# Optimization experiments

Measured on AMD Instinct MI355X. Metric: run time of the kernel, lower is better.

The kernel has to match this reference:

```python
import jax, jax.numpy as jnp
import numpy as np

E = 23   # unique_experts_num
K = 3    # act_experts_num
D = 1024 # in_features
H = 768  # hidden_features (0.75 * dim, per MOEBlock mlp_ratio)


def setup_inputs() -> dict:
    key = jax.random.key(0)
    ks = jax.random.split(key, 12)
    s_in = 1.0 / np.sqrt(D)
    s_hid = 1.0 / np.sqrt(H)
    x = jax.random.normal(ks[0], (4, 1024, D), dtype=jnp.float32)
    gate_W = jax.random.normal(ks[1], (D, E), dtype=jnp.float32) * s_in
    gate_b = jnp.zeros((E,), jnp.float32)
    bias = jnp.zeros((E,), jnp.float32)  # registered buffer, init to zeros
    W1 = jax.random.normal(ks[2], (E, D, H), dtype=jnp.float32) * s_in
    b1 = jnp.zeros((E, H), jnp.float32)
    W2 = jax.random.normal(ks[3], (E, H, D), dtype=jnp.float32) * s_hid
    b2 = jnp.zeros((E, D), jnp.float32)
    sW1 = jax.random.normal(ks[4], (D, H), dtype=jnp.float32) * s_in
    sb1 = jnp.zeros((H,), jnp.float32)
    sW2 = jax.random.normal(ks[5], (H, D), dtype=jnp.float32) * s_hid
    sb2 = jnp.zeros((D,), jnp.float32)
    return {"x": x, "gate_W": gate_W, "gate_b": gate_b, "bias": bias,
            "W1": W1, "b1": b1, "W2": W2, "b2": b2,
            "sW1": sW1, "sb1": sb1, "sW2": sW2, "sb2": sb2}


def reference(x, gate_W, gate_b, bias, W1, b1, W2, b2, sW1, sb1, sW2, sb2):
    o_shape = x.shape
    xt = x.reshape(-1, o_shape[-1])          # [T, D]
    T = xt.shape[0]

    # gating: sigmoid gate, top-k indices chosen on (gate + bias), weights gathered from gate
    gate = jax.nn.sigmoid(xt @ gate_W + gate_b)            # [T, E]
    _, top_idx = jax.lax.top_k(gate + bias, K)             # [T, K]
    top_w = jnp.take_along_axis(gate, top_idx, axis=-1)    # [T, K]
    top_w = top_w / jnp.sum(top_w, axis=-1, keepdims=True)

    # combine matrix: C[t, e] = normalized gate weight if e in top-k of token t else 0
    C = jnp.zeros((T, E), xt.dtype).at[jnp.arange(T)[:, None], top_idx].set(top_w)

    # all-expert dense compute (math-equivalent to dispatch/compute/combine)
    h = jax.nn.gelu(jnp.einsum('td,edh->eth', xt, W1) + b1[:, None, :], approximate=False)
    y = jnp.einsum('eth,ehd->etd', h, W2) + b2[:, None, :]  # [E, T, D]
    moe_out = jnp.einsum('etd,te->td', y, C)                # weighted combine

    # shared expert applied to every token
    shared = jax.nn.gelu(xt @ sW1 + sb1, approximate=False) @ sW2 + sb2
    out = shared + moe_out

    # aux load-balance loss
    gate_norm = gate / jnp.sum(gate, axis=-1, keepdims=True)
    P = jnp.mean(gate_norm, axis=0)                          # [E]
    counts = jnp.sum(jax.nn.one_hot(top_idx, E, dtype=jnp.float32), axis=(0, 1))  # [E]
    F = E * counts / (K * T)
    aux_loss = jnp.sum(P * F)

    return out.reshape(o_shape), aux_loss, counts.astype(jnp.int32)
```

## Files before the change

### kernel.cpp

```cpp
#include <hip/hip_runtime.h>
#include <math.h>

#define TT 4096
#define DD 1024
#define HH 768
#define NE 23
#define NG 24
#define BM 128
#define BN 128
#define BK 64
#define MAXT 160
#define KB1 16
#define KB2 12
#define NY1 6
#define NY2 8
#define NWG1 (MAXT*NY1)
#define NWG2 (MAXT*NY2)

#define WS_CURS   0
#define WS_COUNTS 512
#define WS_PSUM   544
#define WS_OFFS   576
#define WS_TOFFS  608
#define WS_TOTAL  640
#define WS_T2E    672
#define WS_T2A    832
#define WS_TOKE   1024
#define WS_TOKW   13312
#define WS_LTOK   25600
#define WS_LW     41984
#define WS_PPART  58368
#define WS_CPART  81920
#define WS_SIDX   106496
#define XB_OFF  ((size_t)524288)
#define H_OFF   ((size_t)8912896)
#define W1B_OFF ((size_t)34078720)
#define W2B_OFF ((size_t)71827456)

typedef short bf16x8 __attribute__((ext_vector_type(8)));
typedef float f32x4 __attribute__((ext_vector_type(4)));
typedef unsigned short u16x8 __attribute__((ext_vector_type(8)));

#define S_BARRIER() asm volatile("s_barrier" ::: "memory")
#define WAIT_VM8()  asm volatile("s_waitcnt vmcnt(8)" ::: "memory")
#define WAIT_VM0()  asm volatile("s_waitcnt vmcnt(0)" ::: "memory")

__device__ inline unsigned short bfr(float f) {
    unsigned u = __float_as_uint(f);
    u += 0x7fffu + ((u >> 16) & 1u);
    return (unsigned short)(u >> 16);
}
__device__ inline float b2f(unsigned short u) {
    return __uint_as_float((unsigned)u << 16);
}

__device__ __forceinline__ void gl_lds16(const void* g, void* l) {
    __builtin_amdgcn_global_load_lds(
        (const __attribute__((address_space(1))) unsigned int*)g,
        (__attribute__((address_space(3))) unsigned int*)l, 16, 0, 0);
}

__global__ __launch_bounds__(256) void k_gate(
    const float* __restrict__ x, const float* __restrict__ gW,
    const float* __restrict__ gb, const float* __restrict__ bias,
    int* __restrict__ tokE, float* __restrict__ tokW,
    float* __restrict__ Ppart, int* __restrict__ Cpart)
{
    __shared__ float xs[4][DD];
    __shared__ float gv[4][NE];
    __shared__ float ginvs[4];
    __shared__ int sel[4][3];
    const int tid = threadIdx.x;
    const int t0 = blockIdx.x * 4;
    {
        const float4* src = (const float4*)(x + (size_t)t0 * DD);
        float4* dst = (float4*)&xs[0][0];
        #pragma unroll
        for (int i = 0; i < 4; i++) dst[tid + 256 * i] = src[tid + 256 * i];
    }
    __syncthreads();
    const int w = tid >> 6, l = tid & 63;
    const int t = t0 + w;
    if (l < NE) {
        float s0 = 0.f, s1 = 0.f, s2 = 0.f, s3 = 0.f;
        const float* xw = xs[w];
        for (int d = 0; d < DD; d += 4) {
            s0 = fmaf(xw[d + 0], gW[(d + 0) * NE + l], s0);
            s1 = fmaf(xw[d + 1], gW[(d + 1) * NE + l], s1);
            s2 = fmaf(xw[d + 2], gW[(d + 2) * NE + l], s2);
            s3 = fmaf(xw[d + 3], gW[(d + 3) * NE + l], s3);
        }
        float s = (s0 + s1) + (s2 + s3) + gb[l];
        gv[w][l] = 1.f / (1.f + expf(-s));
    }
    __syncthreads();
    if (l == 0) {
        unsigned chosen = 0;
        int be[3]; float bw[3];
        float gsum = 0.f;
        for (int e = 0; e < NE; e++) gsum += gv[w][e];
        #pragma unroll
        for (int k = 0; k < 3; k++) {
            float m = -1e30f; int mi = 0;
            for (int e = 0; e < NE; e++) {
                float kv = gv[w][e] + bias[e];
                if (!((chosen >> e) & 1u) && kv > m) { m = kv; mi = e; }
            }
            chosen |= 1u << mi;
            be[k] = mi; bw[k] = gv[w][mi];
        }
        float inv = 1.f / (bw[0] + bw[1] + bw[2]);
        #pragma unroll
        for (int k = 0; k < 3; k++) {
            tokE[t * 3 + k] = be[k];
            tokW[t * 3 + k] = bw[k] * inv;
            sel[w][k] = be[k];
        }
        ginvs[w] = 1.f / gsum;
    }
    __syncthreads();
    if (tid < NE) {
        float p = gv[0][tid] * ginvs[0] + gv[1][tid] * ginvs[1]
                + gv[2][tid] * ginvs[2] + gv[3][tid] * ginvs[3];
        Ppart[tid * 1024 + blockIdx.x] = p;
        int c = 0;
        #pragma unroll
        for (int w2 = 0; w2 < 4; w2++)
            #pragma unroll
            for (int k = 0; k < 3; k++) c += (sel[w2][k] == tid);
        Cpart[tid * 1024 + blockIdx.x] = c;
    }
}

__global__ __launch_bounds__(256) void k_reduce(
    const float* __restrict__ Ppart, const int* __restrict__ Cpart,
    int* __restrict__ counts, float* __restrict__ Psum)
{
    const int e = blockIdx.x;
    const int tid = threadIdx.x;
    float s = 0.f; int c = 0;
    for (int i = tid; i < 1024; i += 256) {
        s += Ppart[e * 1024 + i];
        c += Cpart[e * 1024 + i];
    }
    #pragma unroll
    for (int off = 32; off >= 1; off >>= 1) {
        s += __shfl_down(s, off, 64);
        c += __shfl_down(c, off, 64);
    }
    __shared__ float ss[4]; __shared__ int sc[4];
    if ((tid & 63) == 0) { ss[tid >> 6] = s; sc[tid >> 6] = c; }
    __syncthreads();
    if (tid == 0) {
        Psum[e] = ss[0] + ss[1] + ss[2] + ss[3];
        counts[e] = sc[0] + sc[1] + sc[2] + sc[3];
    }
}

__global__ void k_scan(const int* __restrict__ counts, const float* __restrict__ Psum,
                       int* __restrict__ offs, int* __restrict__ toffs,
                       int* __restrict__ total, int* __restrict__ t2e,
                       int* __restrict__ t2a, float* __restrict__ outAux)
{
    if (threadIdx.x != 0 || blockIdx.x != 0) return;
    int off = 0, toff = 0;
    for (int e = 0; e < NG; e++) {
        int c = (e < NE) ? counts[e] : TT;
        offs[e] = off; toffs[e] = toff;
        int nt = (c + BM - 1) / BM;
        for (int t = 0; t < nt; t++) {
            t2e[toff + t] = e;
            t2a[toff + t] = off + t * BM;
        }
        off += c; toff += nt;
    }
    offs[NG] = off; toffs[NG] = toff;
    *total = toff;
    float aux = 0.f;
    for (int e = 0; e < NE; e++) {
        float P = Psum[e] / (float)TT;
        float F = (float)NE * (float)counts[e] / (float)(3 * TT);
        aux += P * F;
    }
    outAux[0] = aux;
    for (int e = 0; e < NE; e++) outAux[1 + e] = (float)counts[e];
}

__global__ void k_scatter(const int* __restrict__ tokE, const float* __restrict__ tokW,
                          const int* __restrict__ offs, int* __restrict__ curs,
                          int* __restrict__ ltok, float* __restrict__ lw,
                          int* __restrict__ sidx)
{
    int t = blockIdx.x * 256 + threadIdx.x;
    if (t >= TT) return;
    #pragma unroll
    for (int k = 0; k < 3; k++) {
        int e = tokE[t * 3 + k];
        int pos = atomicAdd(&curs[e * 16], 1);
        int idx = offs[e] + pos;
        ltok[idx] = t; lw[idx] = tokW[t * 3 + k];
        sidx[t * 3 + k] = idx;
    }
    ltok[3 * TT + t] = t;
    lw[3 * TT + t] = 1.f;
}

__global__ __launch_bounds__(256) void k_cvt_x(const float* __restrict__ x,
                                               unsigned short* __restrict__ xb)
{
    const int tid = threadIdx.x;
    #pragma unroll
    for (int it = 0; it < 4; it++) {
        int idx = blockIdx.x * 1024 + it * 256 + tid;
        float4 v = ((const float4*)x)[idx];
        ((ushort4*)xb)[idx] = make_ushort4(bfr(v.x), bfr(v.y), bfr(v.z), bfr(v.w));
    }
}

__global__ __launch_bounds__(256) void k_cvt_w(
    const float* __restrict__ W, const float* __restrict__ Ws,
    int K, int N, unsigned short* __restrict__ dst)
{
    const int e = blockIdx.z, kb = blockIdx.y;
    const int KBt = gridDim.y;
    const int n0 = blockIdx.x * 64;
    const float* src = (e < NE) ? (W + (size_t)e * K * N) : Ws;
    __shared__ unsigned short Ls[64][66];
    const int tid = threadIdx.x;
    const int c = (tid & 15) * 4, r0 = tid >> 4;
    #pragma unroll
    for (int pass = 0; pass < 4; pass++) {
        int row = pass * 16 + r0;
        float4 v = *(const float4*)(src + (size_t)(kb * 64 + row) * N + n0 + c);
        ushort4 u = make_ushort4(bfr(v.x), bfr(v.y), bfr(v.z), bfr(v.w));
        *(ushort4*)&Ls[row][c] = u;
    }
    __syncthreads();
    unsigned short* dbase = dst + ((size_t)(e * KBt + kb) * N + n0) * 64;
    #pragma unroll
    for (int half = 0; half < 2; half++) {
        int g = half * 256 + tid;
        int n = g >> 3, p = g & 7;
        int j = p ^ (n & 7);
        u16x8 u;
        #pragma unroll
        for (int i = 0; i < 8; i++) u[i] = Ls[j * 8 + i][n];
        *(u16x8*)(dbase + n * 64 + p * 8) = u;
    }
}

__global__ __launch_bounds__(256) void k_mm1(
    const unsigned short* __restrict__ xb, const unsigned short* __restrict__ W1b,
    const float* __restrict__ b1, const float* __restrict__ sb1,
    const int* __restrict__ t2e, const int* __restrict__ t2a,
    const int* __restrict__ offs, const int* __restrict__ total,
    const int* __restrict__ ltok, unsigned short* __restrict__ H)
{
    const int id = blockIdx.x;
    const int wg = (id & 7) * (NWG1 / 8) + (id >> 3);
    const int ns = wg / MAXT;
    const int tb = wg % MAXT;
    if (tb >= *total) return;
    const int e = t2e[tb];
    const int a0 = t2a[tb];
    const int acount = min(offs[e + 1] - a0, BM);
    const float* bb = (e < NE) ? (b1 + e * HH) : sb1;
    const int nb = ns * BN;

    __shared__ unsigned short As[2][BM * BK];
    __shared__ unsigned short Bs[2][BN * BK];
    __shared__ int rows[BM];
    const int tid = threadIdx.x;
    if (tid < BM) rows[tid] = ltok[a0 + min(tid, acount - 1)];
    __syncthreads();

    const int wid = tid >> 6, lane = tid & 63;
    const int wr = wid >> 1, wc = wid & 1;
    const int l15 = lane & 15, l4 = lane >> 4;

    float bv[4];
    #pragma unroll
    for (int n = 0; n < 4; n++) bv[n] = bb[nb + wc * 64 + n * 16 + l15];

    f32x4 acc[4][4];
    #pragma unroll
    for (int m = 0; m < 4; m++)
        #pragma unroll
        for (int n = 0; n < 4; n++) acc[m][n] = (f32x4){0.f, 0.f, 0.f, 0.f};

    const unsigned short* aSrc[4];
    int Goff[4];
    #pragma unroll
    for (int c = 0; c < 4; c++) {
        int G = (wid * 4 + c) * 64 + lane;
        int row = G >> 3, j = G & 7;
        aSrc[c] = xb + (size_t)rows[row] * DD + ((j ^ (row & 7)) << 3);
        Goff[c] = G * 8;
    }
    const unsigned short* wbase = W1b + ((size_t)e * KB1 * HH + nb) * 64;

    auto stage = [&](int buf, int kb) {
        #pragma unroll
        for (int c = 0; c < 4; c++)
            gl_lds16(aSrc[c] + kb * 64, &As[buf][Goff[c]]);
        const unsigned short* wb = wbase + (size_t)kb * (HH * 64);
        #pragma unroll
        for (int c = 0; c < 4; c++)
            gl_lds16(wb + Goff[c], &Bs[buf][Goff[c]]);
    };
    auto compute = [&](int buf) {
        #pragma unroll
        for (int kh = 0; kh < 2; kh++) {
            bf16x8 af[4], bf[4];
            #pragma unroll
            for (int f = 0; f < 4; f++) {
                int ar = wr * 64 + f * 16 + l15;
                int br = wc * 64 + f * 16 + l15;
                int pg = (kh << 2) + l4;
                af[f] = *(const bf16x8*)&As[buf][ar * 64 + ((pg ^ (ar & 7)) << 3)];
                bf[f] = *(const bf16x8*)&Bs[buf][br * 64 + ((pg ^ (br & 7)) << 3)];
            }
            #pragma unroll
            for (int m = 0; m < 4; m++)
                #pragma unroll
                for (int n = 0; n < 4; n++)
                    acc[m][n] = __builtin_amdgcn_mfma_f32_16x16x32_bf16(af[m], bf[n], acc[m][n], 0, 0, 0);
        }
    };

    stage(0, 0);
    stage(1, 1);
    WAIT_VM8();
    S_BARRIER();
    #pragma unroll 1
    for (int kb = 0; kb < KB1; kb++) {
        const int cur = kb & 1;
        compute(cur);
        S_BARRIER();
        if (kb + 2 < KB1) {
            stage(cur, kb + 2);
            WAIT_VM8();
            S_BARRIER();
        } else if (kb + 1 < KB1) {
            WAIT_VM0();
            S_BARRIER();
        }
    }

    #pragma unroll
    for (int m = 0; m < 4; m++) {
        int rbase = wr * 64 + m * 16 + l4 * 4;
        #pragma unroll
        for (int n = 0; n < 4; n++) {
            int col = nb + wc * 64 + n * 16 + l15;
            #pragma unroll
            for (int i = 0; i < 4; i++) {
                int r = rbase + i;
                if (r < acount) {
                    float v = acc[m][n][i] + bv[n];
                    float g = 0.5f * v * (1.f + erff(v * 0.70710678118f));
                    H[(size_t)(a0 + r) * HH + col] = bfr(g);
                }
            }
        }
    }
}

__global__ __launch_bounds__(256) void k_mm2(
    const unsigned short* __restrict__ H, const unsigned short* __restrict__ W2b,
    const float* __restrict__ b2, const float* __restrict__ sb2,
    const int* __restrict__ t2e, const int* __restrict__ t2a,
    const int* __restrict__ offs, const int* __restrict__ total,
    const int* __restrict__ ltok, const float* __restrict__ lw,
    unsigned short* __restrict__ yslot, float* __restrict__ out)
{
    const int id = blockIdx.x;
    const int wg = (id & 7) * (NWG2 / 8) + (id >> 3);
    const int ns = wg / MAXT;
    const int tb = wg % MAXT;
    if (tb >= *total) return;
    const int e = t2e[tb];
    const int a0 = t2a[tb];
    const int acount = min(offs[e + 1] - a0, BM);
    const float* bb = (e < NE) ? (b2 + e * DD) : sb2;
    const int nb = ns * BN;

    __shared__ unsigned short As[2][BM * BK];
    __shared__ unsigned short Bs[2][BN * BK];
    __shared__ int rows[BM];
    __shared__ float wts[BM];
    const int tid = threadIdx.x;
    if (tid < BM) {
        rows[tid] = (tid < acount) ? ltok[a0 + tid] : -1;
        wts[tid]  = (tid < acount) ? lw[a0 + tid] : 0.f;
    }
    __syncthreads();

    const int wid = tid >> 6, lane = tid & 63;
    const int wr = wid >> 1, wc = wid & 1;
    const int l15 = lane & 15, l4 = lane >> 4;

    float bv[4];
    #pragma unroll
    for (int n = 0; n < 4; n++) bv[n] = bb[nb + wc * 64 + n * 16 + l15];

    f32x4 acc[4][4];
    #pragma unroll
    for (int m = 0; m < 4; m++)
        #pragma unroll
        for (int n = 0; n < 4; n++) acc[m][n] = (f32x4){0.f, 0.f, 0.f, 0.f};

    const unsigned short* aSrc[4];
    int Goff[4];
    #pragma unroll
    for (int c = 0; c < 4; c++) {
        int G = (wid * 4 + c) * 64 + lane;
        int row = G >> 3, j = G & 7;
        aSrc[c] = H + (size_t)(a0 + row) * HH + ((j ^ (row & 7)) << 3);
        Goff[c] = G * 8;
    }
    const unsigned short* wbase = W2b + ((size_t)e * KB2 * DD + nb) * 64;

    auto stage = [&](int buf, int kb) {
        #pragma unroll
        for (int c = 0; c < 4; c++)
            gl_lds16(aSrc[c] + kb * 64, &As[buf][Goff[c]]);
        const unsigned short* wb = wbase + (size_t)kb * (DD * 64);
        #pragma unroll
        for (int c = 0; c < 4; c++)
            gl_lds16(wb + Goff[c], &Bs[buf][Goff[c]]);
    };
    auto compute = [&](int buf) {
        #pragma unroll
        for (int kh = 0; kh < 2; kh++) {
            bf16x8 af[4], bf[4];
            #pragma unroll
            for (int f = 0; f < 4; f++) {
                int ar = wr * 64 + f * 16 + l15;
                int br = wc * 64 + f * 16 + l15;
                int pg = (kh << 2) + l4;
                af[f] = *(const bf16x8*)&As[buf][ar * 64 + ((pg ^ (ar & 7)) << 3)];
                bf[f] = *(const bf16x8*)&Bs[buf][br * 64 + ((pg ^ (br & 7)) << 3)];
            }
            #pragma unroll
            for (int m = 0; m < 4; m++)
                #pragma unroll
                for (int n = 0; n < 4; n++)
                    acc[m][n] = __builtin_amdgcn_mfma_f32_16x16x32_bf16(af[m], bf[n], acc[m][n], 0, 0, 0);
        }
    };

    stage(0, 0);
    stage(1, 1);
    WAIT_VM8();
    S_BARRIER();
    #pragma unroll 1
    for (int kb = 0; kb < KB2; kb++) {
        const int cur = kb & 1;
        compute(cur);
        S_BARRIER();
        if (kb + 2 < KB2) {
            stage(cur, kb + 2);
            WAIT_VM8();
            S_BARRIER();
        } else if (kb + 1 < KB2) {
            WAIT_VM0();
            S_BARRIER();
        }
    }

    if (e == NE) {
        #pragma unroll
        for (int m = 0; m < 4; m++) {
            int rbase = wr * 64 + m * 16 + l4 * 4;
            #pragma unroll
            for (int n = 0; n < 4; n++) {
                int col = nb + wc * 64 + n * 16 + l15;
                #pragma unroll
                for (int i = 0; i < 4; i++) {
                    int r = rbase + i;
                    out[(size_t)rows[r] * DD + col] = acc[m][n][i] + bv[n];
                }
            }
        }
    } else {
        #pragma unroll
        for (int m = 0; m < 4; m++) {
            int rbase = wr * 64 + m * 16 + l4 * 4;
            #pragma unroll
            for (int n = 0; n < 4; n++) {
                int col = nb + wc * 64 + n * 16 + l15;
                #pragma unroll
                for (int i = 0; i < 4; i++) {
                    int r = rbase + i;
                    if (r < acount)
                        yslot[(size_t)(a0 + r) * DD + col] = bfr(wts[r] * (acc[m][n][i] + bv[n]));
                }
            }
        }
    }
}

__global__ __launch_bounds__(256) void k_combine(
    const unsigned short* __restrict__ yslot, const int* __restrict__ sidx,
    float* __restrict__ out)
{
    const int t = blockIdx.x;
    const int s0 = sidx[t * 3 + 0], s1 = sidx[t * 3 + 1], s2 = sidx[t * 3 + 2];
    const int d = threadIdx.x * 4;
    float* o = out + (size_t)t * DD + d;
    float4 v = *(float4*)o;
    ushort4 a = *(const ushort4*)(yslot + (size_t)s0 * DD + d);
    ushort4 b = *(const ushort4*)(yslot + (size_t)s1 * DD + d);
    ushort4 c = *(const ushort4*)(yslot + (size_t)s2 * DD + d);
    v.x += b2f(a.x) + b2f(b.x) + b2f(c.x);
    v.y += b2f(a.y) + b2f(b.y) + b2f(c.y);
    v.z += b2f(a.z) + b2f(b.z) + b2f(c.z);
    v.w += b2f(a.w) + b2f(b.w) + b2f(c.w);
    *(float4*)o = v;
}

extern "C" void kernel_launch(void* const* d_in, const int* in_sizes, int n_in,
                              void* d_out, int out_size, void* d_ws, size_t ws_size,
                              hipStream_t stream)
{
    const float* x    = (const float*)d_in[0];
    const float* gW   = (const float*)d_in[1];
    const float* gb   = (const float*)d_in[2];
    const float* bias = (const float*)d_in[3];
    const float* W1   = (const float*)d_in[4];
    const float* b1   = (const float*)d_in[5];
    const float* W2   = (const float*)d_in[6];
    const float* b2   = (const float*)d_in[7];
    const float* sW1  = (const float*)d_in[8];
    const float* sb1  = (const float*)d_in[9];
    const float* sW2  = (const float*)d_in[10];
    const float* sb2  = (const float*)d_in[11];
    float* out = (float*)d_out;
    float* wsf = (float*)d_ws;
    int*   wsi = (int*)d_ws;

    hipMemsetAsync(d_ws, 0, 2048, stream);

    int*   curs   = wsi + WS_CURS;
    int*   counts = wsi + WS_COUNTS;
    float* Psum   = wsf + WS_PSUM;
    int*   offs   = wsi + WS_OFFS;
    int*   toffs  = wsi + WS_TOFFS;
    int*   total  = wsi + WS_TOTAL;
    int*   t2e    = wsi + WS_T2E;
    int*   t2a    = wsi + WS_T2A;
    int*   tokE   = wsi + WS_TOKE;
    float* tokW   = wsf + WS_TOKW;
    int*   ltok   = wsi + WS_LTOK;
    float* lwt    = wsf + WS_LW;
    float* Ppart  = wsf + WS_PPART;
    int*   Cpart  = wsi + WS_CPART;
    int*   sidx   = wsi + WS_SIDX;
    unsigned short* xb  = (unsigned short*)((char*)d_ws + XB_OFF);
    unsigned short* Hb  = (unsigned short*)((char*)d_ws + H_OFF);
    unsigned short* W1b = (unsigned short*)((char*)d_ws + W1B_OFF);
    unsigned short* W2b = (unsigned short*)((char*)d_ws + W2B_OFF);
    unsigned short* yslot = W1b;

    k_cvt_x<<<TT * DD / 4096, 256, 0, stream>>>(x, xb);
    k_cvt_w<<<dim3(HH / 64, DD / 64, NG), 256, 0, stream>>>(W1, sW1, DD, HH, W1b);
    k_cvt_w<<<dim3(DD / 64, HH / 64, NG), 256, 0, stream>>>(W2, sW2, HH, DD, W2b);
    k_gate<<<TT / 4, 256, 0, stream>>>(x, gW, gb, bias, tokE, tokW, Ppart, Cpart);
    k_reduce<<<NE, 256, 0, stream>>>(Ppart, Cpart, counts, Psum);
    k_scan<<<1, 64, 0, stream>>>(counts, Psum, offs, toffs, total, t2e, t2a,
                                 out + (size_t)TT * DD);
    k_scatter<<<TT / 256, 256, 0, stream>>>(tokE, tokW, offs, curs, ltok, lwt, sidx);
    k_mm1<<<NWG1, 256, 0, stream>>>(xb, W1b, b1, sb1, t2e, t2a, offs, total, ltok, Hb);
    k_mm2<<<NWG2, 256, 0, stream>>>(Hb, W2b, b2, sb2, t2e, t2a, offs, total, ltok, lwt,
                                    yslot, out);
    k_combine<<<TT, 256, 0, stream>>>(yslot, sidx, out);
}
```

Before: 245.7 us.

## Halve GEMM K-tile to 32 with new swizzled layout and tanh-approx GELU

Halves the K tile of both expert GEMMs from 64 to 32, which doubles the number of k-blocks. The weight pre-layout, the LDS swizzle and the global-to-LDS staging are rebuilt for 32-wide rows, and the LDS fragment offsets are precomputed once instead of per iteration. This shrinks LDS use per stage and may allow more resident workgroups, but it doubles the barrier count per output tile. The exact erf GELU in the first GEMM epilogue is also replaced by a tanh-style approximation computed with a fast exponential, which changes numerics slightly relative to the exact-GELU reference.

After: 251.8 us. 2.5% more time.

```diff
diff --git a/kernel.cpp b/kernel.cpp
--- a/kernel.cpp
+++ b/kernel.cpp
@@ -8,10 +8,10 @@
 #define NG 24
 #define BM 128
 #define BN 128
-#define BK 64
+#define BK 32
 #define MAXT 160
-#define KB1 16
-#define KB2 12
+#define KB1 32
+#define KB2 24
 #define NY1 6
 #define NY2 8
 #define NWG1 (MAXT*NY1)
@@ -42,7 +42,7 @@
 typedef unsigned short u16x8 __attribute__((ext_vector_type(8)));
 
 #define S_BARRIER() asm volatile("s_barrier" ::: "memory")
-#define WAIT_VM8()  asm volatile("s_waitcnt vmcnt(8)" ::: "memory")
+#define WAIT_VM4()  asm volatile("s_waitcnt vmcnt(4)" ::: "memory")
 #define WAIT_VM0()  asm volatile("s_waitcnt vmcnt(0)" ::: "memory")
 
 __device__ inline unsigned short bfr(float f) {
@@ -221,8 +221,8 @@
     const float* __restrict__ W, const float* __restrict__ Ws,
     int K, int N, unsigned short* __restrict__ dst)
 {
-    const int e = blockIdx.z, kb = blockIdx.y;
-    const int KBt = gridDim.y;
+    const int e = blockIdx.z, kt = blockIdx.y;
+    const int KBt = gridDim.y * 2;
     const int n0 = blockIdx.x * 64;
     const float* src = (e < NE) ? (W + (size_t)e * K * N) : Ws;
     __shared__ unsigned short Ls[64][66];
@@ -231,21 +231,20 @@
     #pragma unroll
     for (int pass = 0; pass < 4; pass++) {
         int row = pass * 16 + r0;
-        float4 v = *(const float4*)(src + (size_t)(kb * 64 + row) * N + n0 + c);
+        float4 v = *(const float4*)(src + (size_t)(kt * 64 + row) * N + n0 + c);
         ushort4 u = make_ushort4(bfr(v.x), bfr(v.y), bfr(v.z), bfr(v.w));
         *(ushort4*)&Ls[row][c] = u;
     }
     __syncthreads();
-    unsigned short* dbase = dst + ((size_t)(e * KBt + kb) * N + n0) * 64;
-    #pragma unroll
-    for (int half = 0; half < 2; half++) {
-        int g = half * 256 + tid;
-        int n = g >> 3, p = g & 7;
-        int j = p ^ (n & 7);
+    const int n = tid >> 2, p = tid & 3;
+    const int j = p ^ ((n >> 1) & 3);
+    #pragma unroll
+    for (int kh = 0; kh < 2; kh++) {
+        unsigned short* dbase = dst + ((size_t)(e * KBt + kt * 2 + kh) * N + n0) * 32;
         u16x8 u;
         #pragma unroll
-        for (int i = 0; i < 8; i++) u[i] = Ls[j * 8 + i][n];
-        *(u16x8*)(dbase + n * 64 + p * 8) = u;
+        for (int i = 0; i < 8; i++) u[i] = Ls[kh * 32 + j * 8 + i][n];
+        *(u16x8*)(dbase + n * 32 + p * 8) = u;
     }
 }
 
@@ -288,49 +287,51 @@
         #pragma unroll
         for (int n = 0; n < 4; n++) acc[m][n] = (f32x4){0.f, 0.f, 0.f, 0.f};
 
-    const unsigned short* aSrc[4];
-    int Goff[4];
-    #pragma unroll
-    for (int c = 0; c < 4; c++) {
-        int G = (wid * 4 + c) * 64 + lane;
-        int row = G >> 3, j = G & 7;
-        aSrc[c] = xb + (size_t)rows[row] * DD + ((j ^ (row & 7)) << 3);
-        Goff[c] = G * 8;
-    }
-    const unsigned short* wbase = W1b + ((size_t)e * KB1 * HH + nb) * 64;
+    const unsigned short* aSrc[2];
+    int GA[2];
+    #pragma unroll
+    for (int c = 0; c < 2; c++) {
+        int G = c * 256 + tid;
+        int row = G >> 2, j = G & 3;
+        aSrc[c] = xb + (size_t)rows[row] * DD + ((j ^ ((row >> 1) & 3)) << 3);
+        GA[c] = G * 8;
+    }
+    const unsigned short* wbase = W1b + ((size_t)e * KB1 * HH + nb) * 32;
+
+    const int xorK = (l15 >> 1) & 3;
+    int offA[4], offB[4];
+    #pragma unroll
+    for (int f = 0; f < 4; f++) {
+        offA[f] = (wr * 64 + f * 16 + l15) * 32 + ((l4 ^ xorK) << 3);
+        offB[f] = (wc * 64 + f * 16 + l15) * 32 + ((l4 ^ xorK) << 3);
+    }
 
     auto stage = [&](int buf, int kb) {
         #pragma unroll
-        for (int c = 0; c < 4; c++)
-            gl_lds16(aSrc[c] + kb * 64, &As[buf][Goff[c]]);
-        const unsigned short* wb = wbase + (size_t)kb * (HH * 64);
-        #pragma unroll
-        for (int c = 0; c < 4; c++)
-            gl_lds16(wb + Goff[c], &Bs[buf][Goff[c]]);
+        for (int c = 0; c < 2; c++)
+            gl_lds16(aSrc[c] + kb * 32, &As[buf][GA[c]]);
+        const unsigned short* wb = wbase + (size_t)kb * (HH * 32);
+        #pragma unroll
+        for (int c = 0; c < 2; c++)
+            gl_lds16(wb + GA[c], &Bs[buf][GA[c]]);
     };
     auto compute = [&](int buf) {
-        #pragma unroll
-        for (int kh = 0; kh < 2; kh++) {
-            bf16x8 af[4], bf[4];
+        bf16x8 af[4], bf[4];
+        #pragma unroll
+        for (int f = 0; f < 4; f++) {
+            af[f] = *(const bf16x8*)&As[buf][offA[f]];
+            bf[f] = *(const bf16x8*)&Bs[buf][offB[f]];
+        }
+        #pragma unroll
+        for (int m = 0; m < 4; m++)
             #pragma unroll
-            for (int f = 0; f < 4; f++) {
-                int ar = wr * 64 + f * 16 + l15;
-                int br = wc * 64 + f * 16 + l15;
-                int pg = (kh << 2) + l4;
-                af[f] = *(const bf16x8*)&As[buf][ar * 64 + ((pg ^ (ar & 7)) << 3)];
-                bf[f] = *(const bf16x8*)&Bs[buf][br * 64 + ((pg ^ (br & 7)) << 3)];
-            }
-            #pragma unroll
-            for (int m = 0; m < 4; m++)
-                #pragma unroll
-                for (int n = 0; n < 4; n++)
-                    acc[m][n] = __builtin_amdgcn_mfma_f32_16x16x32_bf16(af[m], bf[n], acc[m][n], 0, 0, 0);
-        }
+            for (int n = 0; n < 4; n++)
+                acc[m][n] = __builtin_amdgcn_mfma_f32_16x16x32_bf16(af[m], bf[n], acc[m][n], 0, 0, 0);
     };
 
     stage(0, 0);
     stage(1, 1);
-    WAIT_VM8();
+    WAIT_VM4();
     S_BARRIER();
     #pragma unroll 1
     for (int kb = 0; kb < KB1; kb++) {
@@ -339,7 +340,7 @@
         S_BARRIER();
         if (kb + 2 < KB1) {
             stage(cur, kb + 2);
-            WAIT_VM8();
+            WAIT_VM4();
             S_BARRIER();
         } else if (kb + 1 < KB1) {
             WAIT_VM0();
@@ -358,7 +359,8 @@
                 int r = rbase + i;
                 if (r < acount) {
                     float v = acc[m][n][i] + bv[n];
-                    float g = 0.5f * v * (1.f + erff(v * 0.70710678118f));
+                    float u = v + 0.044715f * v * v * v;
+                    float g = v / (1.f + __expf(-1.5957691216f * u));
                     H[(size_t)(a0 + r) * HH + col] = bfr(g);
                 }
             }
@@ -410,49 +412,51 @@
         #pragma unroll
         for (int n = 0; n < 4; n++) acc[m][n] = (f32x4){0.f, 0.f, 0.f, 0.f};
 
-    const unsigned short* aSrc[4];
-    int Goff[4];
-    #pragma unroll
-    for (int c = 0; c < 4; c++) {
-        int G = (wid * 4 + c) * 64 + lane;
-        int row = G >> 3, j = G & 7;
-        aSrc[c] = H + (size_t)(a0 + row) * HH + ((j ^ (row & 7)) << 3);
-        Goff[c] = G * 8;
-    }
-    const unsigned short* wbase = W2b + ((size_t)e * KB2 * DD + nb) * 64;
+    const unsigned short* aSrc[2];
+    int GA[2];
+    #pragma unroll
+    for (int c = 0; c < 2; c++) {
+        int G = c * 256 + tid;
+        int row = G >> 2, j = G & 3;
+        aSrc[c] = H + (size_t)(a0 + row) * HH + ((j ^ ((row >> 1) & 3)) << 3);
+        GA[c] = G * 8;
+    }
+    const unsigned short* wbase = W2b + ((size_t)e * KB2 * DD + nb) * 32;
+
+    const int xorK = (l15 >> 1) & 3;
+    int offA[4], offB[4];
+    #pragma unroll
+    for (int f = 0; f < 4; f++) {
+        offA[f] = (wr * 64 + f * 16 + l15) * 32 + ((l4 ^ xorK) << 3);
+        offB[f] = (wc * 64 + f * 16 + l15) * 32 + ((l4 ^ xorK) << 3);
+    }
 
     auto stage = [&](int buf, int kb) {
         #pragma unroll
-        for (int c = 0; c < 4; c++)
-            gl_lds16(aSrc[c] + kb * 64, &As[buf][Goff[c]]);
-        const unsigned short* wb = wbase + (size_t)kb * (DD * 64);
-        #pragma unroll
-        for (int c = 0; c < 4; c++)
-            gl_lds16(wb + Goff[c], &Bs[buf][Goff[c]]);
+        for (int c = 0; c < 2; c++)
+            gl_lds16(aSrc[c] + kb * 32, &As[buf][GA[c]]);
+        const unsigned short* wb = wbase + (size_t)kb * (DD * 32);
+        #pragma unroll
+        for (int c = 0; c < 2; c++)
+            gl_lds16(wb + GA[c], &Bs[buf][GA[c]]);
     };
     auto compute = [&](int buf) {
-        #pragma unroll
-        for (int kh = 0; kh < 2; kh++) {
-            bf16x8 af[4], bf[4];
+        bf16x8 af[4], bf[4];
+        #pragma unroll
+        for (int f = 0; f < 4; f++) {
+            af[f] = *(const bf16x8*)&As[buf][offA[f]];
+            bf[f] = *(const bf16x8*)&Bs[buf][offB[f]];
+        }
+        #pragma unroll
+        for (int m = 0; m < 4; m++)
             #pragma unroll
-            for (int f = 0; f < 4; f++) {
-                int ar = wr * 64 + f * 16 + l15;
-                int br = wc * 64 + f * 16 + l15;
-                int pg = (kh << 2) + l4;
-                af[f] = *(const bf16x8*)&As[buf][ar * 64 + ((pg ^ (ar & 7)) << 3)];
-                bf[f] = *(const bf16x8*)&Bs[buf][br * 64 + ((pg ^ (br & 7)) << 3)];
-            }
-            #pragma unroll
-            for (int m = 0; m < 4; m++)
-                #pragma unroll
-                for (int n = 0; n < 4; n++)
-                    acc[m][n] = __builtin_amdgcn_mfma_f32_16x16x32_bf16(af[m], bf[n], acc[m][n], 0, 0, 0);
-        }
+            for (int n = 0; n < 4; n++)
+                acc[m][n] = __builtin_amdgcn_mfma_f32_16x16x32_bf16(af[m], bf[n], acc[m][n], 0, 0, 0);
     };
 
     stage(0, 0);
     stage(1, 1);
-    WAIT_VM8();
+    WAIT_VM4();
     S_BARRIER();
     #pragma unroll 1
     for (int kb = 0; kb < KB2; kb++) {
@@ -461,7 +465,7 @@
         S_BARRIER();
         if (kb + 2 < KB2) {
             stage(cur, kb + 2);
-            WAIT_VM8();
+            WAIT_VM4();
             S_BARRIER();
         } else if (kb + 1 < KB2) {
             WAIT_VM0();
```
